# Performance work log

Hardware: AMD Instinct MI355X
Metric: run time of the kernel (lower is better)

The kernel has to match this reference:

```python
import jax, jax.numpy as jnp
import numpy as np

MAX_NORM = 1.0 - 1e-5  # Poincare ball (c=1) boundary clip, geoopt-style
NUM_HEADS = 8

def _norm(x):
    return jnp.sqrt(jnp.sum(x * x, axis=-1, keepdims=True) + 1e-30)

def projx(x):
    n = _norm(x)
    return jnp.where(n > MAX_NORM, x * (MAX_NORM / n), x)

def expmap0(u):
    n = _norm(u)
    return jnp.tanh(n) * u / n

def logmap0(x):
    n = _norm(x)
    return jnp.arctanh(jnp.minimum(n, MAX_NORM)) * x / n

def mobius_add(x, y):
    xy = jnp.sum(x * y, axis=-1, keepdims=True)
    x2 = jnp.sum(x * x, axis=-1, keepdims=True)
    y2 = jnp.sum(y * y, axis=-1, keepdims=True)
    num = (1.0 + 2.0 * xy + y2) * x + (1.0 - x2) * y
    den = 1.0 + 2.0 * xy + x2 * y2
    return num / jnp.maximum(den, 1e-15)

def mobius_matvec(M, x):
    xn = _norm(x)
    mx = x @ M.T
    mxn = _norm(mx)
    return jnp.tanh(mxn / xn * jnp.arctanh(jnp.minimum(xn, MAX_NORM))) * mx / mxn

def man_linear(x, W, b):
    # Manifold_Linear: mobius matvec + mobius bias add + project (geoopt MobiusLinear)
    return projx(mobius_add(mobius_matvec(W, x), b))

def mob_relu(x):
    # Mob_Act(ReLU): act in tangent space at origin
    return projx(expmap0(jax.nn.relu(logmap0(x))))

def layer_norm(x, g, b):
    mu = jnp.mean(x, axis=-1, keepdims=True)
    v = jnp.var(x, axis=-1, keepdims=True)
    return (x - mu) / jnp.sqrt(v + 1e-5) * g + b

def mha_tan_space(x_q, x_kv, Wq, bq, Wk, bk, Wv, bv, Wo, bo, num_heads):
    # ManifoldMHA with att_metric='tan_space': manifold linear projections,
    # scaled dot-product attention in the tangent space at the origin.
    q = logmap0(man_linear(x_q, Wq, bq))   # (S, B, E)
    k = logmap0(man_linear(x_kv, Wk, bk))  # (T, B, E)
    v = logmap0(man_linear(x_kv, Wv, bv))  # (T, B, E)
    S, B, E = q.shape
    hd = E // num_heads
    def split(t):  # (T,B,E) -> (B,H,T,hd)
        return t.reshape(t.shape[0], B, num_heads, hd).transpose(1, 2, 0, 3)
    qh, kh, vh = split(q), split(k), split(v)
    scores = jnp.einsum('bhqd,bhkd->bhqk', qh, kh) / np.sqrt(hd).astype(np.float32)
    attn = jax.nn.softmax(scores, axis=-1)
    o = jnp.einsum('bhqk,bhkd->bhqd', attn, vh)  # (B,H,S,hd)
    o = o.transpose(2, 0, 1, 3).reshape(S, B, E)
    o = expmap0(o)
    return man_linear(o, Wo, bo)

def forward_block(x, ln1_g, ln1_b, ln2_g, ln2_b, Wq, bq, Wk, bk, Wv, bv, Wo, bo, W1, b1, W2, b2):
    residual = x
    h = expmap0(layer_norm(logmap0(x), ln1_g, ln1_b))
    h = mha_tan_space(h, h, Wq, bq, Wk, bk, Wv, bv, Wo, bo, NUM_HEADS)
    h = projx(h)
    h = projx(mobius_add(h, residual))
    residual = h
    h = projx(expmap0(layer_norm(logmap0(h), ln2_g, ln2_b)))
    h = mob_relu(man_linear(h, W1, b1))   # fc1 = Manifold_Linear + Mob_Act
    h = projx(h)                          # act_dropout (identity, eval) + projx
    h = mob_relu(man_linear(h, W2, b2))   # fc2
    h = projx(mobius_add(h, residual))
    return h

def setup_inputs() -> dict:
    key = jax.random.key(0)
    ks = jax.random.split(key, 18)
    S, B, E, F = 128, 256, 512, 2048
    sE = 1.0 / np.sqrt(E)
    sF = 1.0 / np.sqrt(F)
    # input points must lie inside the unit ball: randn scaled small
    x = jax.random.normal(ks[0], (S, B, E), jnp.float32) * 0.02
    def w(k, o, i, s):
        return jax.random.normal(k, (o, i), jnp.float32) * s
    def bias(k, d):
        return jax.random.normal(k, (d,), jnp.float32) * 1e-3
    return {
        'x': x,
        'ln1_g': jnp.ones((E,), jnp.float32), 'ln1_b': jnp.zeros((E,), jnp.float32),
        'ln2_g': jnp.ones((E,), jnp.float32), 'ln2_b': jnp.zeros((E,), jnp.float32),
        'Wq': w(ks[1], E, E, sE), 'bq': bias(ks[2], E),
        'Wk': w(ks[3], E, E, sE), 'bk': bias(ks[4], E),
        'Wv': w(ks[5], E, E, sE), 'bv': bias(ks[6], E),
        'Wo': w(ks[7], E, E, sE), 'bo': bias(ks[8], E),
        'W1': w(ks[9], F, E, sE), 'b1': bias(ks[10], F),
        'W2': w(ks[11], E, F, sF), 'b2': bias(ks[12], E),
    }

def reference(x, ln1_g, ln1_b, ln2_g, ln2_b, Wq, bq, Wk, bk, Wv, bv, Wo, bo, W1, b1, W2, b2):
    return forward_block(x, ln1_g, ln1_b, ln2_g, ln2_b, Wq, bq, Wk, bk, Wv, bv, Wo, bo, W1, b1, W2, b2)
```

## Files before the change

kernel.cpp:

```cpp
#include <hip/hip_runtime.h>
#include <math.h>

#define S_DIM 128
#define B_DIM 256
#define E_DIM 512
#define F_DIM 2048
#define N_ROWS (S_DIM * B_DIM)
#define CH 8192
#define MAXN 0.99999f

typedef __bf16 bf16x8 __attribute__((ext_vector_type(8)));
typedef float f32x4 __attribute__((ext_vector_type(4)));

__device__ __forceinline__ float frcp(float x) { return __builtin_amdgcn_rcpf(x); }
__device__ __forceinline__ float frsq(float x) { return __builtin_amdgcn_rsqf(x); }
__device__ __forceinline__ float fexp2(float x) { return __builtin_amdgcn_exp2f(x); }
__device__ __forceinline__ float flog2(float x) { return __builtin_amdgcn_logf(x); }
__device__ __forceinline__ float fatanh(float x) {
  return 0.34657359f * flog2((1.f + x) * frcp(1.f - x));
}
__device__ __forceinline__ float ftanh(float x) {
  float t = fexp2(x * -2.88539008f);
  return (1.f - t) * frcp(1.f + t);
}

__device__ __forceinline__ ushort f2bf(float f) {
  __bf16 h = (__bf16)f;
  return __builtin_bit_cast(ushort, h);
}
__device__ __forceinline__ uint pack2(float a, float b) {
  return (uint)f2bf(a) | ((uint)f2bf(b) << 16);
}
__device__ __forceinline__ void ldbf8(const ushort* p, float (&f)[8]) {
  uint4 u = *reinterpret_cast<const uint4*>(p);
  f[0] = __uint_as_float(u.x << 16);
  f[1] = __uint_as_float(u.x & 0xFFFF0000u);
  f[2] = __uint_as_float(u.y << 16);
  f[3] = __uint_as_float(u.y & 0xFFFF0000u);
  f[4] = __uint_as_float(u.z << 16);
  f[5] = __uint_as_float(u.z & 0xFFFF0000u);
  f[6] = __uint_as_float(u.w << 16);
  f[7] = __uint_as_float(u.w & 0xFFFF0000u);
}

__device__ __forceinline__ void gld16(const ushort* g, ushort* l) {
  __builtin_amdgcn_global_load_lds(
      (const __attribute__((address_space(1))) void*)g,
      (__attribute__((address_space(3))) void*)l, 16, 0, 0);
}

template <int K>
__device__ __forceinline__ void waveRed(float (&v)[K]) {
#pragma unroll
  for (int o = 1; o < 64; o <<= 1) {
#pragma unroll
    for (int i = 0; i < K; ++i) v[i] += __shfl_xor(v[i], o);
  }
}

__global__ __launch_bounds__(256) void k_f2bf(const float* __restrict__ in,
                                              ushort* __restrict__ out, int n) {
  for (int i = blockIdx.x * 256 + threadIdx.x; i < n; i += gridDim.x * 256)
    out[i] = f2bf(in[i]);
}

__global__ void k_bsums(const float* __restrict__ bq, const float* __restrict__ bk,
                        const float* __restrict__ bv, const float* __restrict__ g1,
                        const float* __restrict__ lb1, float* __restrict__ bs) {
  int lane = threadIdx.x;
  float p[6];
#pragma unroll
  for (int i = 0; i < 6; ++i) p[i] = 0.f;
  for (int i = lane; i < E_DIM; i += 64) {
    float a = bq[i]; p[0] += a * a;
    a = bk[i]; p[1] += a * a;
    a = bv[i]; p[2] += a * a;
    float g = g1[i], l = lb1[i];
    p[3] += g * g; p[4] += g * l; p[5] += l * l;
  }
  waveRed<6>(p);
  if (lane == 0) {
    bs[0] = p[0]; bs[1] = p[1]; bs[2] = p[2];
    bs[7] = p[3]; bs[8] = p[4]; bs[9] = p[5];
  }
}

__global__ __launch_bounds__(256) void k_stage1(
    const float* __restrict__ x, const float* __restrict__ g,
    const float* __restrict__ bb, const float* __restrict__ bs,
    ushort* __restrict__ h, float* __restrict__ hn) {
  int wv = threadIdx.x >> 6, lane = threadIdx.x & 63;
  int row = blockIdx.x * 8 + wv * 2;
  size_t base = (size_t)row * E_DIM + lane * 8;
  float v[2][8], gv[8], bv[8];
  *(float4*)&v[0][0] = *(const float4*)(x + base);
  *(float4*)&v[0][4] = *(const float4*)(x + base + 4);
  *(float4*)&v[1][0] = *(const float4*)(x + base + E_DIM);
  *(float4*)&v[1][4] = *(const float4*)(x + base + E_DIM + 4);
  *(float4*)&gv[0] = *(const float4*)(g + lane * 8);
  *(float4*)&gv[4] = *(const float4*)(g + lane * 8 + 4);
  *(float4*)&bv[0] = *(const float4*)(bb + lane * 8);
  *(float4*)&bv[4] = *(const float4*)(bb + lane * 8 + 4);
  float s[10];
#pragma unroll
  for (int i = 0; i < 10; ++i) s[i] = 0.f;
#pragma unroll
  for (int i = 0; i < 8; ++i) {
    float gg = gv[i] * gv[i], gb = gv[i] * bv[i];
#pragma unroll
    for (int r2 = 0; r2 < 2; ++r2) {
      float vv = v[r2][i];
      s[r2 * 5 + 0] += vv * vv;
      s[r2 * 5 + 1] += vv;
      s[r2 * 5 + 2] += vv * vv * gg;
      s[r2 * 5 + 3] += vv * gg;
      s[r2 * 5 + 4] += vv * gb;
    }
  }
  waveRed<10>(s);
  float Sg2 = bs[7], Sgb = bs[8], Sb2 = bs[9];
#pragma unroll
  for (int r2 = 0; r2 < 2; ++r2) {
    float T0 = s[r2 * 5 + 0], T1 = s[r2 * 5 + 1], T2 = s[r2 * 5 + 2];
    float T3 = s[r2 * 5 + 3], T4 = s[r2 * 5 + 4];
    float se = T0 + 1e-30f;
    float rn = frsq(se);
    float n = se * rn;
    float a = fatanh(fminf(n, MAXN)) * rn;
    float mu = a * T1 * (1.f / 512.f);
    float var = fmaxf(a * a * T0 * (1.f / 512.f) - mu * mu, 0.f);
    float rstd = frsq(var + 1e-5f);
    float A = a * rstd, B = -mu * rstd;
    float se2 = fmaxf(A * A * T2 + 2.f * A * B * T3 + 2.f * A * T4 +
                          B * B * Sg2 + 2.f * B * Sgb + Sb2, 0.f) + 1e-30f;
    float rn2 = frsq(se2);
    float n2 = se2 * rn2;
    float th = ftanh(n2);
    float f = th * rn2;
    float e[8];
#pragma unroll
    for (int i = 0; i < 8; ++i) e[i] = (A * v[r2][i] + B) * gv[i] + bv[i];
    uint4 o = {pack2(e[0] * f, e[1] * f), pack2(e[2] * f, e[3] * f),
               pack2(e[4] * f, e[5] * f), pack2(e[6] * f, e[7] * f)};
    *reinterpret_cast<uint4*>(h + base + r2 * E_DIM) = o;
    if (lane == 0) hn[row + r2] = th;
  }
}

__global__ __launch_bounds__(256) void k_gemm_bf16(
    const ushort* __restrict__ A, const ushort* __restrict__ B,
    float* __restrict__ C, int K, int M, int kseg,
    unsigned long long partStride, int obf, int GX, int GY) {
  __shared__ __align__(16) ushort As[2][128 * 32];
  __shared__ __align__(16) ushort Bs[2][128 * 32];
  int b = blockIdx.x;
  int rx = b & 7, kk2 = b >> 3;
  int bx = kk2 % GX;
  int gg = rx + 8 * (kk2 / GX);
  int by = gg % GY, bz = gg / GY;
  int tid = threadIdx.x;
  int w = tid >> 6, lane = tid & 63;
  int wm = w >> 1, wn = w & 1;
  size_t row0 = (size_t)by * 128;
  size_t col0 = (size_t)bx * 128;
  int k0 = bz * kseg;

  const ushort* gA =
      A + (row0 + w * 32 + (lane >> 2)) * (size_t)K + (lane & 3) * 8 + k0;
  const ushort* gB =
      B + (col0 + w * 32 + (lane >> 2)) * (size_t)K + (lane & 3) * 8 + k0;
  const int lofs = (w * 32) * 32;
  const int rowK16 = 16 * K;
  int fro = (lane & 15) * 32 + (lane >> 4) * 8;

  f32x4 zero = {0.f, 0.f, 0.f, 0.f};
  f32x4 acc[4][4];
#pragma unroll
  for (int i = 0; i < 4; ++i)
#pragma unroll
    for (int j = 0; j < 4; ++j) acc[i][j] = zero;

  gld16(gA, As[0] + lofs);
  gld16(gA + rowK16, As[0] + lofs + 16 * 32);
  gld16(gB, Bs[0] + lofs);
  gld16(gB + rowK16, Bs[0] + lofs + 16 * 32);
  asm volatile("s_waitcnt vmcnt(0)" ::: "memory");
  __builtin_amdgcn_s_barrier();
  __builtin_amdgcn_sched_barrier(0);

  int cur = 0;
  for (int kt = 0; kt < kseg; kt += 32) {
    if (kt + 32 < kseg) {
      int nxt = cur ^ 1;
      gld16(gA + kt + 32, As[nxt] + lofs);
      gld16(gA + kt + 32 + rowK16, As[nxt] + lofs + 16 * 32);
      gld16(gB + kt + 32, Bs[nxt] + lofs);
      gld16(gB + kt + 32 + rowK16, Bs[nxt] + lofs + 16 * 32);
    }
    const ushort* raA = As[cur] + (wm * 64) * 32 + fro;
    const ushort* raB = Bs[cur] + (wn * 64) * 32 + fro;
    bf16x8 af[4], bfv[4];
#pragma unroll
    for (int t = 0; t < 4; ++t) {
      af[t] = *reinterpret_cast<const bf16x8*>(raA + t * 512);
      bfv[t] = *reinterpret_cast<const bf16x8*>(raB + t * 512);
    }
#pragma unroll
    for (int i = 0; i < 4; ++i)
#pragma unroll
      for (int j = 0; j < 4; ++j)
        acc[i][j] = __builtin_amdgcn_mfma_f32_16x16x32_bf16(af[i], bfv[j],
                                                            acc[i][j], 0, 0, 0);
    asm volatile("s_waitcnt vmcnt(0)" ::: "memory");
    __builtin_amdgcn_s_barrier();
    __builtin_amdgcn_sched_barrier(0);
    cur ^= 1;
  }

  int crow = wm * 64 + (lane >> 4) * 4;
  int ccol = (int)col0 + wn * 64 + (lane & 15);
  if (obf) {
    ushort* Cu = (ushort*)C;
#pragma unroll
    for (int ti = 0; ti < 4; ++ti) {
      size_t r = row0 + crow + ti * 16;
#pragma unroll
      for (int tj = 0; tj < 4; ++tj) {
        int cc = ccol + tj * 16;
#pragma unroll
        for (int reg = 0; reg < 4; ++reg)
          Cu[(r + reg) * (size_t)M + cc] = f2bf(acc[ti][tj][reg]);
      }
    }
  } else {
    float* Cz = C + (size_t)bz * partStride;
#pragma unroll
    for (int ti = 0; ti < 4; ++ti) {
      size_t r = row0 + crow + ti * 16;
#pragma unroll
      for (int tj = 0; tj < 4; ++tj) {
        int cc = ccol + tj * 16;
#pragma unroll
        for (int reg = 0; reg < 4; ++reg)
          Cz[(r + reg) * (size_t)M + cc] = acc[ti][tj][reg];
      }
    }
  }
}

__global__ __launch_bounds__(256) void k_epi_qkv(const ushort* __restrict__ mx,
                                                 const float* __restrict__ xn_arr,
                                                 const float* __restrict__ bias,
                                                 const float* __restrict__ bs_sb2,
                                                 ushort* __restrict__ qout) {
  int wv = threadIdx.x >> 6, lane = threadIdx.x & 63;
  int row = blockIdx.x * 8 + wv * 2;
  size_t base = (size_t)row * E_DIM + lane * 8;
  float m[2][8], bv[8];
  ldbf8(mx + base, m[0]);
  ldbf8(mx + base + E_DIM, m[1]);
  *(float4*)&bv[0] = *(const float4*)(bias + lane * 8);
  *(float4*)&bv[4] = *(const float4*)(bias + lane * 8 + 4);
  float s[4];
#pragma unroll
  for (int i = 0; i < 4; ++i) s[i] = 0.f;
#pragma unroll
  for (int i = 0; i < 8; ++i) {
#pragma unroll
    for (int r2 = 0; r2 < 2; ++r2) {
      s[r2 * 2 + 0] += m[r2][i] * m[r2][i];
      s[r2 * 2 + 1] += m[r2][i] * bv[i];
    }
  }
  waveRed<4>(s);
  float S2 = *bs_sb2;
#pragma unroll
  for (int r2 = 0; r2 < 2; ++r2) {
    float S0 = s[r2 * 2 + 0], S1 = s[r2 * 2 + 1];
    float se = S0 + 1e-30f;
    float rmx = frsq(se);
    float mxn = se * rmx;
    float xn = xn_arr[row + r2];
    float aa = fatanh(fminf(xn, MAXN));
    float tt = ftanh(mxn * frcp(xn) * aa);
    float c = tt * rmx;
    float xy = c * S1, y2 = S2, x2 = tt * tt;
    float c1 = 1.f + 2.f * xy + y2, c2 = 1.f - x2;
    float iden = frcp(fmaxf(1.f + 2.f * xy + x2 * y2, 1e-15f));
    float cc1 = c1 * c * iden, cc2 = c2 * iden;
    float un2 = fmaxf(cc1 * cc1 * S0 + 2.f * cc1 * cc2 * S1 + cc2 * cc2 * S2, 0.f);
    float ue = un2 + 1e-30f;
    float run = frsq(ue);
    float un = ue * run;
    float ne = fminf(un, MAXN);
    float f = fatanh(ne) * run;
    float u[8];
#pragma unroll
    for (int i = 0; i < 8; ++i) u[i] = (cc1 * m[r2][i] + cc2 * bv[i]) * f;
    uint4 o = {pack2(u[0], u[1]), pack2(u[2], u[3]), pack2(u[4], u[5]),
               pack2(u[6], u[7])};
    *reinterpret_cast<uint4*>(qout + base + r2 * E_DIM) = o;
  }
}

__global__ __launch_bounds__(256) void k_attn(const ushort* __restrict__ q,
                                              const ushort* __restrict__ k,
                                              const ushort* __restrict__ v,
                                              ushort* __restrict__ o) {
  __shared__ __align__(16) ushort smem[27136];
  ushort* Qs = smem;
  ushort* Ks = smem + 9216;
  ushort* VTs = smem + 18432;
  ushort* Ps = smem;
  int bh = blockIdx.x;
  int b = bh >> 3, h = bh & 7;
  int tid = threadIdx.x;
  int w = tid >> 6, lane = tid & 63;
  const size_t BE = (size_t)B_DIM * E_DIM;
  size_t gbase = (size_t)b * E_DIM + (size_t)h * 64;

  {
    int s = tid >> 1, half = (tid & 1) * 32;
    const ushort* qr = q + gbase + (size_t)s * BE + half;
    const ushort* kr = k + gbase + (size_t)s * BE + half;
    const ushort* vr = v + gbase + (size_t)s * BE + half;
#pragma unroll
    for (int j = 0; j < 4; ++j) {
      *reinterpret_cast<uint4*>(&Qs[s * 72 + half + j * 8]) =
          *reinterpret_cast<const uint4*>(qr + j * 8);
      *reinterpret_cast<uint4*>(&Ks[s * 72 + half + j * 8]) =
          *reinterpret_cast<const uint4*>(kr + j * 8);
    }
    ushort tv[32];
#pragma unroll
    for (int j = 0; j < 4; ++j)
      *reinterpret_cast<uint4*>(&tv[j * 8]) =
          *reinterpret_cast<const uint4*>(vr + j * 8);
#pragma unroll
    for (int d = 0; d < 32; ++d) VTs[(half + d) * 136 + s] = tv[d];
  }
  __syncthreads();

  f32x4 zero = {0.f, 0.f, 0.f, 0.f};
  f32x4 sacc[2][8];
#pragma unroll
  for (int i = 0; i < 2; ++i)
#pragma unroll
    for (int j = 0; j < 8; ++j) sacc[i][j] = zero;
  {
    const ushort* qb = Qs + (w * 32 + (lane & 15)) * 72 + (lane >> 4) * 8;
    const ushort* kb = Ks + (lane & 15) * 72 + (lane >> 4) * 8;
#pragma unroll
    for (int kk = 0; kk < 2; ++kk) {
      bf16x8 a0 = *reinterpret_cast<const bf16x8*>(qb + kk * 32);
      bf16x8 a1 = *reinterpret_cast<const bf16x8*>(qb + 16 * 72 + kk * 32);
#pragma unroll
      for (int tj = 0; tj < 8; ++tj) {
        bf16x8 bf = *reinterpret_cast<const bf16x8*>(kb + tj * 16 * 72 + kk * 32);
        sacc[0][tj] = __builtin_amdgcn_mfma_f32_16x16x32_bf16(a0, bf,
                                                              sacc[0][tj], 0, 0, 0);
        sacc[1][tj] = __builtin_amdgcn_mfma_f32_16x16x32_bf16(a1, bf,
                                                              sacc[1][tj], 0, 0, 0);
      }
    }
  }

#pragma unroll
  for (int ti = 0; ti < 2; ++ti) {
#pragma unroll
    for (int r = 0; r < 4; ++r) {
      float mx = -1e30f;
#pragma unroll
      for (int tj = 0; tj < 8; ++tj) mx = fmaxf(mx, sacc[ti][tj][r]);
      mx = fmaxf(mx, __shfl_xor(mx, 1));
      mx = fmaxf(mx, __shfl_xor(mx, 2));
      mx = fmaxf(mx, __shfl_xor(mx, 4));
      mx = fmaxf(mx, __shfl_xor(mx, 8));
      float l = 0.f;
#pragma unroll
      for (int tj = 0; tj < 8; ++tj) {
        float e = fexp2((sacc[ti][tj][r] - mx) * (0.125f * 1.44269504f));
        sacc[ti][tj][r] = e;
        l += e;
      }
      l += __shfl_xor(l, 1);
      l += __shfl_xor(l, 2);
      l += __shfl_xor(l, 4);
      l += __shfl_xor(l, 8);
      float inv = frcp(l);
#pragma unroll
      for (int tj = 0; tj < 8; ++tj) sacc[ti][tj][r] *= inv;
    }
  }

  __syncthreads();
  {
    int qr0 = w * 32 + (lane >> 4) * 4;
    int kc = lane & 15;
#pragma unroll
    for (int ti = 0; ti < 2; ++ti)
#pragma unroll
      for (int tj = 0; tj < 8; ++tj)
#pragma unroll
        for (int r = 0; r < 4; ++r)
          Ps[(qr0 + ti * 16 + r) * 136 + tj * 16 + kc] =
              f2bf(sacc[ti][tj][r]);
  }
  __syncthreads();

  f32x4 oacc[2][4];
#pragma unroll
  for (int i = 0; i < 2; ++i)
#pragma unroll
    for (int j = 0; j < 4; ++j) oacc[i][j] = zero;
  {
    const ushort* pb = Ps + (w * 32 + (lane & 15)) * 136 + (lane >> 4) * 8;
    const ushort* vb = VTs + (lane & 15) * 136 + (lane >> 4) * 8;
#pragma unroll
    for (int kk = 0; kk < 4; ++kk) {
      bf16x8 a0 = *reinterpret_cast<const bf16x8*>(pb + kk * 32);
      bf16x8 a1 = *reinterpret_cast<const bf16x8*>(pb + 16 * 136 + kk * 32);
#pragma unroll
      for (int tj = 0; tj < 4; ++tj) {
        bf16x8 bv = *reinterpret_cast<const bf16x8*>(vb + tj * 16 * 136 + kk * 32);
        oacc[0][tj] = __builtin_amdgcn_mfma_f32_16x16x32_bf16(a0, bv,
                                                              oacc[0][tj], 0, 0, 0);
        oacc[1][tj] = __builtin_amdgcn_mfma_f32_16x16x32_bf16(a1, bv,
                                                              oacc[1][tj], 0, 0, 0);
      }
    }
  }

  {
    int qr0 = w * 32 + (lane >> 4) * 4;
    int dc = lane & 15;
#pragma unroll
    for (int ti = 0; ti < 2; ++ti)
#pragma unroll
      for (int tj = 0; tj < 4; ++tj)
#pragma unroll
        for (int r = 0; r < 4; ++r)
          o[(size_t)(qr0 + ti * 16 + r) * BE + gbase + tj * 16 + dc] =
              f2bf(oacc[ti][tj][r]);
  }
}

__global__ __launch_bounds__(256) void k_expmap_rows(const ushort* __restrict__ in,
                                                     ushort* __restrict__ out,
                                                     float* __restrict__ nrm) {
  int wv = threadIdx.x >> 6, lane = threadIdx.x & 63;
  int row = blockIdx.x * 8 + wv * 2;
  size_t base = (size_t)row * E_DIM + lane * 8;
  float v[2][8];
  ldbf8(in + base, v[0]);
  ldbf8(in + base + E_DIM, v[1]);
  float s[2] = {0.f, 0.f};
#pragma unroll
  for (int i = 0; i < 8; ++i) {
    s[0] += v[0][i] * v[0][i];
    s[1] += v[1][i] * v[1][i];
  }
  waveRed<2>(s);
#pragma unroll
  for (int r2 = 0; r2 < 2; ++r2) {
    float se = s[r2] + 1e-30f;
    float rn = frsq(se);
    float n = se * rn;
    float th = ftanh(n);
    float f = th * rn;
    uint4 o = {pack2(v[r2][0] * f, v[r2][1] * f), pack2(v[r2][2] * f, v[r2][3] * f),
               pack2(v[r2][4] * f, v[r2][5] * f), pack2(v[r2][6] * f, v[r2][7] * f)};
    *reinterpret_cast<uint4*>(out + base + r2 * E_DIM) = o;
    if (lane == 0) nrm[row + r2] = th;
  }
}

__global__ __launch_bounds__(256) void k_epi_attnout(
    const ushort* __restrict__ mo, const float* __restrict__ xn_arr,
    const float* __restrict__ bo, const float* __restrict__ xin,
    const float* __restrict__ g2, const float* __restrict__ b2,
    ushort* __restrict__ h2, float* __restrict__ h2n,
    ushort* __restrict__ r2o) {
  int row = blockIdx.x * 4 + (threadIdx.x >> 6);
  int lane = threadIdx.x & 63;
  size_t base = (size_t)row * E_DIM + lane * 8;
  float m[8], bv[8];
  ldbf8(mo + base, m);
  *(float4*)&bv[0] = *(const float4*)(bo + lane * 8);
  *(float4*)&bv[4] = *(const float4*)(bo + lane * 8 + 4);
  float s[5] = {0.f, 0.f, 0.f, 0.f, 0.f};
#pragma unroll
  for (int i = 0; i < 8; ++i) {
    s[0] += m[i] * m[i]; s[1] += m[i] * bv[i]; s[2] += bv[i] * bv[i];
    s[3] += m[i]; s[4] += bv[i];
  }
  waveRed<5>(s);
  float se = s[0] + 1e-30f;
  float rmx = frsq(se);
  float mxn = se * rmx;
  float xn = xn_arr[row];
  float aa = fatanh(fminf(xn, MAXN));
  float tt = ftanh(mxn * frcp(xn) * aa);
  float c = tt * rmx;
  float xy = c * s[1], y2 = s[2], x2 = tt * tt;
  float c1 = 1.f + 2.f * xy + y2, c2 = 1.f - x2;
  float iden = frcp(fmaxf(1.f + 2.f * xy + x2 * y2, 1e-15f));
  float cc1 = c1 * c * iden, cc2 = c2 * iden;
  float un2 = fmaxf(cc1 * cc1 * s[0] + 2.f * cc1 * cc2 * s[1] + cc2 * cc2 * s[2], 0.f);
  float ue = un2 + 1e-30f;
  float run = frsq(ue);
  float un = ue * run;
  float ps = un > MAXN ? MAXN * run : 1.f;
  float zn = fminf(un, MAXN);
  float z[8];
#pragma unroll
  for (int i = 0; i < 8; ++i) z[i] = (cc1 * m[i] + cc2 * bv[i]) * ps;
  float sumz = ps * (cc1 * s[3] + cc2 * s[4]);
  float r[8];
  *(float4*)&r[0] = *(const float4*)(xin + base);
  *(float4*)&r[4] = *(const float4*)(xin + base + 4);
  float t2[3] = {0.f, 0.f, 0.f};
#pragma unroll
  for (int i = 0; i < 8; ++i) {
    t2[0] += z[i] * r[i]; t2[1] += r[i] * r[i]; t2[2] += r[i];
  }
  waveRed<3>(t2);
  float xy2 = t2[0], y22 = t2[1], x22 = zn * zn;
  float d1 = 1.f + 2.f * xy2 + y22, d2 = 1.f - x22;
  float iden2 = frcp(fmaxf(1.f + 2.f * xy2 + x22 * y22, 1e-15f));
  float wn2 = fmaxf(iden2 * iden2 *
                        (d1 * d1 * x22 + 2.f * d1 * d2 * xy2 + d2 * d2 * y22),
                    0.f);
  float we = wn2 + 1e-30f;
  float rwn = frsq(we);
  float wn = we * rwn;
  float ps2 = wn > MAXN ? MAXN * rwn : 1.f;
  float w[8];
#pragma unroll
  for (int i = 0; i < 8; ++i) w[i] = (d1 * z[i] + d2 * r[i]) * iden2 * ps2;
  uint4 ro = {pack2(w[0], w[1]), pack2(w[2], w[3]), pack2(w[4], w[5]),
              pack2(w[6], w[7])};
  *reinterpret_cast<uint4*>(r2o + base) = ro;
  float ne = fminf(wn, MAXN);
  float ath = fatanh(ne);
  float lf = ath * frcp(ne);
  float sumw = ps2 * iden2 * (d1 * sumz + d2 * t2[2]);
  float mu = lf * sumw * (1.f / 512.f);
  float var = fmaxf(ath * ath * (1.f / 512.f) - mu * mu, 0.f);
  float rstd = frsq(var + 1e-5f);
  float gv[8], b2v[8];
  *(float4*)&gv[0] = *(const float4*)(g2 + lane * 8);
  *(float4*)&gv[4] = *(const float4*)(g2 + lane * 8 + 4);
  *(float4*)&b2v[0] = *(const float4*)(b2 + lane * 8);
  *(float4*)&b2v[4] = *(const float4*)(b2 + lane * 8 + 4);
  float e[8];
  float s3[1] = {0.f};
#pragma unroll
  for (int i = 0; i < 8; ++i) {
    e[i] = (lf * w[i] - mu) * rstd * gv[i] + b2v[i];
    s3[0] += e[i] * e[i];
  }
  waveRed<1>(s3);
  float s3e = s3[0] + 1e-30f;
  float rn3 = frsq(s3e);
  float n3 = s3e * rn3;
  float en = ftanh(n3);
  float f = en * rn3;
  if (en > MAXN) f *= MAXN * frcp(en);
  uint4 o = {pack2(e[0] * f, e[1] * f), pack2(e[2] * f, e[3] * f),
             pack2(e[4] * f, e[5] * f), pack2(e[6] * f, e[7] * f)};
  *reinterpret_cast<uint4*>(h2 + base) = o;
  if (lane == 0) h2n[row] = fminf(en, MAXN);
}

__global__ __launch_bounds__(256) void k_epi_ffn1(const ushort* __restrict__ mr_,
                                                  const float* __restrict__ xn_arr,
                                                  const float* __restrict__ bias,
                                                  ushort* __restrict__ hid,
                                                  float* __restrict__ hn_out) {
  int wv = threadIdx.x >> 6, lane = threadIdx.x & 63;
  int row = blockIdx.x * 8 + wv * 2;
  const ushort* mr = mr_ + (size_t)row * F_DIM + lane * 32;
  const float* br = bias + lane * 32;
  float m[2][32], bv[32];
#pragma unroll
  for (int j = 0; j < 4; ++j) {
    ldbf8(mr + j * 8, *(float(*)[8])&m[0][j * 8]);
    ldbf8(mr + F_DIM + j * 8, *(float(*)[8])&m[1][j * 8]);
  }
#pragma unroll
  for (int j = 0; j < 8; ++j)
    *(float4*)&bv[j * 4] = *(const float4*)(br + j * 4);
  float s[5];
#pragma unroll
  for (int i = 0; i < 5; ++i) s[i] = 0.f;
#pragma unroll
  for (int i = 0; i < 32; ++i) {
#pragma unroll
    for (int r2 = 0; r2 < 2; ++r2) {
      s[r2 * 2 + 0] += m[r2][i] * m[r2][i];
      s[r2 * 2 + 1] += m[r2][i] * bv[i];
    }
    s[4] += bv[i] * bv[i];
  }
  waveRed<5>(s);
  float s2[2] = {0.f, 0.f};
#pragma unroll
  for (int r2 = 0; r2 < 2; ++r2) {
    float S0 = s[r2 * 2 + 0], S1 = s[r2 * 2 + 1], S2 = s[4];
    float se = S0 + 1e-30f;
    float rmx = frsq(se);
    float mxn = se * rmx;
    float xn = xn_arr[row + r2];
    float aa = fatanh(fminf(xn, MAXN));
    float tt = ftanh(mxn * frcp(xn) * aa);
    float c = tt * rmx;
    float xy = c * S1, y2 = S2, x2 = tt * tt;
    float c1 = 1.f + 2.f * xy + y2, c2 = 1.f - x2;
    float iden = frcp(fmaxf(1.f + 2.f * xy + x2 * y2, 1e-15f));
    float cc1 = c1 * c * iden, cc2 = c2 * iden;
    float un2 = fmaxf(cc1 * cc1 * S0 + 2.f * cc1 * cc2 * S1 + cc2 * cc2 * S2, 0.f);
    float ue = un2 + 1e-30f;
    float run = frsq(ue);
    float un = ue * run;
    float zn = fminf(un, MAXN);
    float lf = fatanh(zn) * run;
#pragma unroll
    for (int i = 0; i < 32; ++i) {
      m[r2][i] = fmaxf((cc1 * m[r2][i] + cc2 * bv[i]) * lf, 0.f);
      s2[r2] += m[r2][i] * m[r2][i];
    }
  }
  waveRed<2>(s2);
#pragma unroll
  for (int r2 = 0; r2 < 2; ++r2) {
    float s2e = s2[r2] + 1e-30f;
    float rrn = frsq(s2e);
    float rn = s2e * rrn;
    float en = ftanh(rn);
    float f = en * rrn;
    if (en > MAXN) f *= MAXN * frcp(en);
    ushort* hr = hid + (size_t)(row + r2) * F_DIM + lane * 32;
#pragma unroll
    for (int j = 0; j < 4; ++j) {
      uint4 o = {pack2(m[r2][j * 8 + 0] * f, m[r2][j * 8 + 1] * f),
                 pack2(m[r2][j * 8 + 2] * f, m[r2][j * 8 + 3] * f),
                 pack2(m[r2][j * 8 + 4] * f, m[r2][j * 8 + 5] * f),
                 pack2(m[r2][j * 8 + 6] * f, m[r2][j * 8 + 7] * f)};
      *reinterpret_cast<uint4*>(hr + j * 8) = o;
    }
    if (lane == 0) hn_out[row + r2] = fminf(en, MAXN);
  }
}

__global__ __launch_bounds__(256) void k_epi_final(
    const float* __restrict__ m2, const float* __restrict__ xn_arr,
    const float* __restrict__ bias, const ushort* __restrict__ res,
    float* __restrict__ out) {
  int wv = threadIdx.x >> 6, lane = threadIdx.x & 63;
  int row = blockIdx.x * 8 + wv * 2;
  size_t base = (size_t)row * E_DIM + lane * 8;
  const size_t P2 = (size_t)CH * E_DIM;
  float m[2][8], bv[8], q[2][8];
#pragma unroll
  for (int r2 = 0; r2 < 2; ++r2) {
    float ta[8], tb[8];
    *(float4*)&ta[0] = *(const float4*)(m2 + base + r2 * E_DIM);
    *(float4*)&ta[4] = *(const float4*)(m2 + base + r2 * E_DIM + 4);
    *(float4*)&tb[0] = *(const float4*)(m2 + P2 + base + r2 * E_DIM);
    *(float4*)&tb[4] = *(const float4*)(m2 + P2 + base + r2 * E_DIM + 4);
#pragma unroll
    for (int i = 0; i < 8; ++i) m[r2][i] = ta[i] + tb[i];
    ldbf8(res + base + r2 * E_DIM, q[r2]);
  }
  *(float4*)&bv[0] = *(const float4*)(bias + lane * 8);
  *(float4*)&bv[4] = *(const float4*)(bias + lane * 8 + 4);
  float s[7];
#pragma unroll
  for (int i = 0; i < 7; ++i) s[i] = 0.f;
#pragma unroll
  for (int i = 0; i < 8; ++i) {
#pragma unroll
    for (int r2 = 0; r2 < 2; ++r2) {
      s[r2 * 3 + 0] += m[r2][i] * m[r2][i];
      s[r2 * 3 + 1] += m[r2][i] * bv[i];
      s[r2 * 3 + 2] += q[r2][i] * q[r2][i];
    }
    s[6] += bv[i] * bv[i];
  }
  waveRed<7>(s);
  float r[2][8];
  float s2[4];
#pragma unroll
  for (int i = 0; i < 4; ++i) s2[i] = 0.f;
#pragma unroll
  for (int r2 = 0; r2 < 2; ++r2) {
    float S0 = s[r2 * 3 + 0], S1 = s[r2 * 3 + 1], S2 = s[6];
    float se = S0 + 1e-30f;
    float rmx = frsq(se);
    float mxn = se * rmx;
    float xn = xn_arr[row + r2];
    float aa = fatanh(fminf(xn, MAXN));
    float tt = ftanh(mxn * frcp(xn) * aa);
    float c = tt * rmx;
    float xy = c * S1, y2 = S2, x2 = tt * tt;
    float c1 = 1.f + 2.f * xy + y2, c2 = 1.f - x2;
    float iden = frcp(fmaxf(1.f + 2.f * xy + x2 * y2, 1e-15f));
    float cc1 = c1 * c * iden, cc2 = c2 * iden;
    float un2 = fmaxf(cc1 * cc1 * S0 + 2.f * cc1 * cc2 * S1 + cc2 * cc2 * S2, 0.f);
    float ue = un2 + 1e-30f;
    float run = frsq(ue);
    float un = ue * run;
    float zn = fminf(un, MAXN);
    float lf = fatanh(zn) * run;
#pragma unroll
    for (int i = 0; i < 8; ++i) {
      r[r2][i] = fmaxf((cc1 * m[r2][i] + cc2 * bv[i]) * lf, 0.f);
      s2[r2 * 2 + 0] += r[r2][i] * r[r2][i];
      s2[r2 * 2 + 1] += r[r2][i] * q[r2][i];
    }
  }
  waveRed<4>(s2);
#pragma unroll
  for (int r2 = 0; r2 < 2; ++r2) {
    float s2e = s2[r2 * 2 + 0] + 1e-30f;
    float rrn = frsq(s2e);
    float rn = s2e * rrn;
    float en = ftanh(rn);
    float f = en * rrn;
    if (en > MAXN) f *= MAXN * frcp(en);
    float hn = fminf(en, MAXN);
    float xy2 = f * s2[r2 * 2 + 1], y22 = s[r2 * 3 + 2], x22 = hn * hn;
    float d1 = 1.f + 2.f * xy2 + y22, d2 = 1.f - x22;
    float iden2 = frcp(fmaxf(1.f + 2.f * xy2 + x22 * y22, 1e-15f));
    float wn2 = fmaxf(iden2 * iden2 *
                          (d1 * d1 * x22 + 2.f * d1 * d2 * xy2 + d2 * d2 * y22),
                      0.f);
    float we = wn2 + 1e-30f;
    float rwn = frsq(we);
    float wn = we * rwn;
    float ps2 = wn > MAXN ? MAXN * rwn : 1.f;
    float w[8];
#pragma unroll
    for (int i = 0; i < 8; ++i)
      w[i] = (d1 * r[r2][i] * f + d2 * q[r2][i]) * iden2 * ps2;
    *(float4*)(out + base + r2 * E_DIM) = *(float4*)&w[0];
    *(float4*)(out + base + r2 * E_DIM + 4) = *(float4*)&w[4];
  }
}

extern "C" void kernel_launch(void* const* d_in, const int* in_sizes, int n_in,
                              void* d_out, int out_size, void* d_ws,
                              size_t ws_size, hipStream_t stream) {
  const float* x   = (const float*)d_in[0];
  const float* g1  = (const float*)d_in[1];
  const float* lb1 = (const float*)d_in[2];
  const float* g2  = (const float*)d_in[3];
  const float* lb2 = (const float*)d_in[4];
  const float* Wq  = (const float*)d_in[5];
  const float* bq  = (const float*)d_in[6];
  const float* Wk  = (const float*)d_in[7];
  const float* bk  = (const float*)d_in[8];
  const float* Wv  = (const float*)d_in[9];
  const float* bv  = (const float*)d_in[10];
  const float* Wo  = (const float*)d_in[11];
  const float* bo  = (const float*)d_in[12];
  const float* W1  = (const float*)d_in[13];
  const float* b1  = (const float*)d_in[14];
  const float* W2  = (const float*)d_in[15];
  const float* b2  = (const float*)d_in[16];
  float* out = (float*)d_out;
  float* ws = (float*)d_ws;

  const size_t NE = (size_t)N_ROWS * E_DIM;
  const size_t WF = (4 * (size_t)E_DIM * E_DIM +
                     2 * (size_t)F_DIM * E_DIM) / 2;
  ushort* Cb   = (ushort*)ws;
  ushort* r2u  = (ushort*)(ws + NE / 2);
  float* R_a = ws + NE;
  float* R_q = ws + NE + NE / 2;
  float* R_k = ws + 2 * NE;
  float* R_v = ws + 2 * NE + NE / 2;
  ushort* wqb = (ushort*)(ws + 3 * NE);
  ushort* wkb = wqb + (size_t)E_DIM * E_DIM;
  ushort* wvb = wkb + (size_t)E_DIM * E_DIM;
  ushort* wob = wvb + (size_t)E_DIM * E_DIM;
  ushort* w1b = wob + (size_t)E_DIM * E_DIM;
  ushort* w2b = w1b + (size_t)F_DIM * E_DIM;
  float* n_h1 = ws + 3 * NE + WF;
  float* n_oe = n_h1 + N_ROWS;
  float* n_h2 = n_oe + N_ROWS;
  float* n_h3 = n_h2 + N_ROWS;
  float* bs = n_h3 + N_ROWS;
  const size_t need = (3 * NE + WF + 4 * (size_t)N_ROWS + 16) * sizeof(float);
  if (ws_size < need) return;

  k_bsums<<<1, 64, 0, stream>>>(bq, bk, bv, g1, lb1, bs);
  k_f2bf<<<256, 256, 0, stream>>>(Wq, wqb, E_DIM * E_DIM);
  k_f2bf<<<256, 256, 0, stream>>>(Wk, wkb, E_DIM * E_DIM);
  k_f2bf<<<256, 256, 0, stream>>>(Wv, wvb, E_DIM * E_DIM);
  k_f2bf<<<256, 256, 0, stream>>>(Wo, wob, E_DIM * E_DIM);
  k_f2bf<<<512, 256, 0, stream>>>(W1, w1b, F_DIM * E_DIM);
  k_f2bf<<<512, 256, 0, stream>>>(W2, w2b, F_DIM * E_DIM);

  ushort* h1b = (ushort*)R_a;
  ushort* qb = (ushort*)R_q;
  ushort* kb = (ushort*)R_k;
  ushort* vb = (ushort*)R_v;

  k_stage1<<<N_ROWS / 8, 256, 0, stream>>>(x, g1, lb1, bs, h1b, n_h1);
  const int gE = 4 * 256;
  k_gemm_bf16<<<gE, 256, 0, stream>>>(h1b, wqb, (float*)Cb, E_DIM, E_DIM,
                                      E_DIM, 0, 1, 4, 256);
  k_epi_qkv<<<N_ROWS / 8, 256, 0, stream>>>(Cb, n_h1, bq, bs + 0, qb);
  k_gemm_bf16<<<gE, 256, 0, stream>>>(h1b, wkb, (float*)Cb, E_DIM, E_DIM,
                                      E_DIM, 0, 1, 4, 256);
  k_epi_qkv<<<N_ROWS / 8, 256, 0, stream>>>(Cb, n_h1, bk, bs + 1, kb);
  k_gemm_bf16<<<gE, 256, 0, stream>>>(h1b, wvb, (float*)Cb, E_DIM, E_DIM,
                                      E_DIM, 0, 1, 4, 256);
  k_epi_qkv<<<N_ROWS / 8, 256, 0, stream>>>(Cb, n_h1, bv, bs + 2, vb);

  k_attn<<<B_DIM * 8, 256, 0, stream>>>(qb, kb, vb, Cb);
  ushort* oeb = (ushort*)R_a;
  k_expmap_rows<<<N_ROWS / 8, 256, 0, stream>>>(Cb, oeb, n_oe);

  ushort* h2b = (ushort*)R_a;
  k_gemm_bf16<<<gE, 256, 0, stream>>>(oeb, wob, (float*)Cb, E_DIM, E_DIM,
                                      E_DIM, 0, 1, 4, 256);
  k_epi_attnout<<<N_ROWS / 4, 256, 0, stream>>>(Cb, n_oe, bo, x, g2, lb2,
                                                h2b, n_h2, r2u);

  ushort* m1 = Cb;
  ushort* hidb = (ushort*)R_v;
  float* m2 = R_q;
  for (int c = 0; c < N_ROWS / CH; ++c) {
    size_t ro = (size_t)c * CH;
    k_gemm_bf16<<<16 * 64, 256, 0, stream>>>(
        h2b + ro * E_DIM, w1b, (float*)m1, E_DIM, F_DIM, E_DIM, 0, 1, 16, 64);
    k_epi_ffn1<<<CH / 8, 256, 0, stream>>>(m1, n_h2 + ro, b1, hidb, n_h3 + ro);
    k_gemm_bf16<<<4 * 64 * 2, 256, 0, stream>>>(
        hidb, w2b, m2, F_DIM, E_DIM, F_DIM / 2,
        (unsigned long long)((size_t)CH * E_DIM), 0, 4, 64);
    k_epi_final<<<CH / 8, 256, 0, stream>>>(m2, n_h3 + ro, b2,
                                            r2u + ro * E_DIM, out + ro * E_DIM);
  }
}
```

Measured before the change: 762.9 us.

## Write QKV in head-major layout and drop split-K for FFN2 GEMM

The QKV epilogue now writes q/k/v directly in a (B,H,S,hd) head-contiguous layout, so the attention kernel loads each head's tile with fully contiguous 16-byte reads instead of strided rows. Separately, the second FFN GEMM no longer uses split-K with two fp32 partial buffers. It runs a single full-K pass writing bf16 output, which the final epilogue reads directly. This cuts fp32 partial traffic and the summation step but halves the FFN2 grid, which may reduce occupancy, and it rounds the FFN2 output to bf16.

```diff
diff --git a/kernel.cpp b/kernel.cpp
--- a/kernel.cpp
+++ b/kernel.cpp
@@ -274,6 +274,7 @@
   }
   waveRed<4>(s);
   float S2 = *bs_sb2;
+  int hh = lane >> 3, dd = (lane & 7) * 8;
 #pragma unroll
   for (int r2 = 0; r2 < 2; ++r2) {
     float S0 = s[r2 * 2 + 0], S1 = s[r2 * 2 + 1];
@@ -299,7 +300,10 @@
     for (int i = 0; i < 8; ++i) u[i] = (cc1 * m[r2][i] + cc2 * bv[i]) * f;
     uint4 o = {pack2(u[0], u[1]), pack2(u[2], u[3]), pack2(u[4], u[5]),
                pack2(u[6], u[7])};
-    *reinterpret_cast<uint4*>(qout + base + r2 * E_DIM) = o;
+    int rr = row + r2;
+    int sS = rr >> 8, bB = rr & 255;
+    ushort* dst = qout + ((size_t)(bB * 8 + hh) * S_DIM + sS) * 64 + dd;
+    *reinterpret_cast<uint4*>(dst) = o;
   }
 }
 
@@ -320,24 +324,22 @@
   size_t gbase = (size_t)b * E_DIM + (size_t)h * 64;
 
   {
-    int s = tid >> 1, half = (tid & 1) * 32;
-    const ushort* qr = q + gbase + (size_t)s * BE + half;
-    const ushort* kr = k + gbase + (size_t)s * BE + half;
-    const ushort* vr = v + gbase + (size_t)s * BE + half;
-#pragma unroll
-    for (int j = 0; j < 4; ++j) {
-      *reinterpret_cast<uint4*>(&Qs[s * 72 + half + j * 8]) =
-          *reinterpret_cast<const uint4*>(qr + j * 8);
-      *reinterpret_cast<uint4*>(&Ks[s * 72 + half + j * 8]) =
-          *reinterpret_cast<const uint4*>(kr + j * 8);
-    }
-    ushort tv[32];
-#pragma unroll
-    for (int j = 0; j < 4; ++j)
-      *reinterpret_cast<uint4*>(&tv[j * 8]) =
-          *reinterpret_cast<const uint4*>(vr + j * 8);
-#pragma unroll
-    for (int d = 0; d < 32; ++d) VTs[(half + d) * 136 + s] = tv[d];
+    const ushort* qs = q + (size_t)bh * (S_DIM * 64);
+    const ushort* ks = k + (size_t)bh * (S_DIM * 64);
+    const ushort* vs = v + (size_t)bh * (S_DIM * 64);
+#pragma unroll
+    for (int it = 0; it < 4; ++it) {
+      int g = tid * 8 + it * 2048;
+      int s = g >> 6, c = g & 63;
+      *reinterpret_cast<uint4*>(&Qs[s * 72 + c]) =
+          *reinterpret_cast<const uint4*>(qs + g);
+      *reinterpret_cast<uint4*>(&Ks[s * 72 + c]) =
+          *reinterpret_cast<const uint4*>(ks + g);
+      ushort tv[8];
+      *reinterpret_cast<uint4*>(tv) = *reinterpret_cast<const uint4*>(vs + g);
+#pragma unroll
+      for (int j = 0; j < 8; ++j) VTs[(c + j) * 136 + s] = tv[j];
+    }
   }
   __syncthreads();
 
@@ -654,23 +656,16 @@
 }
 
 __global__ __launch_bounds__(256) void k_epi_final(
-    const float* __restrict__ m2, const float* __restrict__ xn_arr,
+    const ushort* __restrict__ m2, const float* __restrict__ xn_arr,
     const float* __restrict__ bias, const ushort* __restrict__ res,
     float* __restrict__ out) {
   int wv = threadIdx.x >> 6, lane = threadIdx.x & 63;
   int row = blockIdx.x * 8 + wv * 2;
   size_t base = (size_t)row * E_DIM + lane * 8;
-  const size_t P2 = (size_t)CH * E_DIM;
   float m[2][8], bv[8], q[2][8];
 #pragma unroll
   for (int r2 = 0; r2 < 2; ++r2) {
-    float ta[8], tb[8];
-    *(float4*)&ta[0] = *(const float4*)(m2 + base + r2 * E_DIM);
-    *(float4*)&ta[4] = *(const float4*)(m2 + base + r2 * E_DIM + 4);
-    *(float4*)&tb[0] = *(const float4*)(m2 + P2 + base + r2 * E_DIM);
-    *(float4*)&tb[4] = *(const float4*)(m2 + P2 + base + r2 * E_DIM + 4);
-#pragma unroll
-    for (int i = 0; i < 8; ++i) m[r2][i] = ta[i] + tb[i];
+    ldbf8(m2 + base + r2 * E_DIM, m[r2]);
     ldbf8(res + base + r2 * E_DIM, q[r2]);
   }
   *(float4*)&bv[0] = *(const float4*)(bias + lane * 8);
@@ -832,16 +827,15 @@
 
   ushort* m1 = Cb;
   ushort* hidb = (ushort*)R_v;
-  float* m2 = R_q;
+  ushort* m2u = (ushort*)R_q;
   for (int c = 0; c < N_ROWS / CH; ++c) {
     size_t ro = (size_t)c * CH;
     k_gemm_bf16<<<16 * 64, 256, 0, stream>>>(
         h2b + ro * E_DIM, w1b, (float*)m1, E_DIM, F_DIM, E_DIM, 0, 1, 16, 64);
     k_epi_ffn1<<<CH / 8, 256, 0, stream>>>(m1, n_h2 + ro, b1, hidb, n_h3 + ro);
-    k_gemm_bf16<<<4 * 64 * 2, 256, 0, stream>>>(
-        hidb, w2b, m2, F_DIM, E_DIM, F_DIM / 2,
-        (unsigned long long)((size_t)CH * E_DIM), 0, 4, 64);
-    k_epi_final<<<CH / 8, 256, 0, stream>>>(m2, n_h3 + ro, b2,
+    k_gemm_bf16<<<4 * 64, 256, 0, stream>>>(
+        hidb, w2b, (float*)m2u, F_DIM, E_DIM, F_DIM, 0, 1, 4, 64);
+    k_epi_final<<<CH / 8, 256, 0, stream>>>(m2u, n_h3 + ro, b2,
                                             r2u + ro * E_DIM, out + ro * E_DIM);
   }
 }
```

After: 800.2 us. +4.9%, slower.
